# Kernel optimization log

Measured on AMD Instinct MI355X. Metric: run time of the kernel, lower is better.

Reference implementation:

```python
import jax, jax.numpy as jnp
import numpy as np

B, S, HID, H = 2, 2048, 1024, 16
D_HEAD = HID // H  # 64
EPS = 1e-5


def _gammas():
    lo, hi = np.log(1.0 / 512.0), np.log(1.0 / 32.0)
    return (1.0 - np.exp(np.linspace(lo, hi, H))).astype(np.float32)


def _decay_mask():
    # D[h, n, m] = gamma_h^(n-m) for n >= m else 0  (causal exponential decay)
    gam = jnp.asarray(_gammas())                      # [H]
    pos = jnp.arange(S, dtype=jnp.float32)
    diff = pos[:, None] - pos[None, :]                # [S, S]
    keep = diff >= 0
    logg = jnp.log(gam)[:, None, None]                # [H,1,1]
    safe = jnp.where(keep, diff, 0.0)[None]           # avoid inf for masked entries
    return jnp.where(keep[None], jnp.exp(safe * logg), 0.0)  # [H, S, S]


def setup_inputs() -> dict:
    key = jax.random.key(0)
    ks = jax.random.split(key, 10)
    rn = lambda k, shape, s=1.0: jax.random.normal(k, shape, dtype=jnp.float32) * s
    return {
        "x": rn(ks[0], (B, S, HID)),
        "wq": rn(ks[1], (H, D_HEAD, D_HEAD), 1.0 / np.sqrt(D_HEAD)),
        "bq": rn(ks[2], (H, D_HEAD), 0.02),
        "wk": rn(ks[3], (H, D_HEAD, D_HEAD), 1.0 / np.sqrt(D_HEAD)),
        "bk": rn(ks[4], (H, D_HEAD), 0.02),
        "wv": rn(ks[5], (H, D_HEAD, D_HEAD), 1.0 / np.sqrt(D_HEAD)),
        "theta": rn(ks[6], (H, D_HEAD), 1.0 / D_HEAD),
        "gn_weight": jnp.ones((HID,), jnp.float32),
        "gn_bias": jnp.zeros((HID,), jnp.float32),
        "weight1": rn(ks[7], (HID, HID), 1.0 / HID),
        "weight2": rn(ks[8], (HID, HID), 1.0 / HID),
    }


def reference(x, wq, bq, wk, bk, wv, theta, gn_weight, gn_bias, weight1, weight2):
    # Per-head retention (all heads vectorized; torch loops over heads).
    xh = x.reshape(B, S, H, D_HEAD)
    q = jnp.einsum('bshd,hde->bshe', xh, wq) + bq
    k = jnp.einsum('bshd,hde->bshe', xh, wk) + bk
    v = jnp.einsum('bshd,hde->bshe', xh, wv)
    # Complex rotary factors exp(i*n*theta) on q, conj on k -> real part of q k^H:
    ang = jnp.arange(S, dtype=jnp.float32)[:, None, None] * theta[None]  # [S,H,d]
    cs, sn = jnp.cos(ang), jnp.sin(ang)
    scores = (jnp.einsum('bshd,bthd->bhst', q * cs, k * cs)
              + jnp.einsum('bshd,bthd->bhst', q * sn, k * sn))  # Re(QK^H) [B,H,S,S]
    scores = scores * _decay_mask()[None]                        # decay mask
    ret = jnp.einsum('bhst,bthd->bshd', scores, v)               # [B,S,H,d]
    # GroupNorm with groups = n_heads over channels (per-head normalization).
    mean = jnp.mean(ret, axis=-1, keepdims=True)
    var = jnp.var(ret, axis=-1, keepdims=True)
    retn = (ret - mean) * jax.lax.rsqrt(var + EPS)
    retn = retn.reshape(B, S, HID) * gn_weight + gn_bias
    # Swish gate on x @ W1, residual add, project with W2.
    gate = x @ weight1
    out = gate * jax.nn.sigmoid(gate) + retn
    return out @ weight2
```

## Files before the change

### kernel.cpp

```cpp
#include <hip/hip_runtime.h>
#include <cstdint>
#include <cstddef>

#define B_ 2
#define S_ 2048
#define HID_ 1024
#define H_ 16
#define DH_ 64

typedef __attribute__((ext_vector_type(8))) short short8;
typedef __attribute__((ext_vector_type(8))) unsigned short ushort8;
typedef __attribute__((ext_vector_type(4))) unsigned short ushort4v;
typedef __attribute__((ext_vector_type(4))) float floatx4;
typedef __attribute__((ext_vector_type(4))) float float4v;

static __device__ __forceinline__ unsigned short f2bf(float f) {
  unsigned int u = __float_as_uint(f);
  u += 0x7fffu + ((u >> 16) & 1u);
  return (unsigned short)(u >> 16);
}
static __device__ __forceinline__ float bf2f(unsigned short h) {
  return __uint_as_float(((unsigned int)h) << 16);
}

__global__ __launch_bounds__(256) void convert_kernel(
    const float* __restrict__ x, const float* __restrict__ w1,
    const float* __restrict__ w2, unsigned short* __restrict__ x_bf,
    unsigned short* __restrict__ w1t, unsigned short* __restrict__ w2t_hi,
    unsigned short* __restrict__ w2t_lo) {
  const int NX = B_ * S_ * HID_;
  const int NW = HID_ * HID_;
  int idx = blockIdx.x * 256 + threadIdx.x;
  if (idx < NX) {
    x_bf[idx] = f2bf(x[idx]);
  } else if (idx < NX + NW) {
    int i = idx - NX;
    int n = i >> 10, k = i & 1023;
    w1t[i] = f2bf(w1[k * HID_ + n]);
  } else if (idx < NX + 2 * NW) {
    int i = idx - NX - NW;
    int n = i >> 10, k = i & 1023;
    float v = w2[k * HID_ + n];
    unsigned short h = f2bf(v);
    w2t_hi[i] = h;
    w2t_lo[i] = f2bf(v - bf2f(h));
  }
}

__global__ __launch_bounds__(256) void qkv_kernel(
    const float* __restrict__ x, const float* __restrict__ wq,
    const float* __restrict__ bq, const float* __restrict__ wk,
    const float* __restrict__ bk, const float* __restrict__ wv,
    const float* __restrict__ theta,
    unsigned short* __restrict__ q_h, unsigned short* __restrict__ q_l,
    unsigned short* __restrict__ k_h, unsigned short* __restrict__ k_l,
    unsigned short* __restrict__ v_th, unsigned short* __restrict__ v_tl,
    int b) {
  __shared__ __align__(16) float xs[64 * 68];
  __shared__ __align__(16) float wqs[64 * 68];
  __shared__ __align__(16) float wks[64 * 68];
  __shared__ __align__(16) float wvs[64 * 68];

  int tid = threadIdx.x;
  int st = blockIdx.x, h = blockIdx.y;
  int s0 = st * 64;

#pragma unroll
  for (int i = 0; i < 4; ++i) {
    int cid = tid + i * 256;
    int r = cid >> 4, c4 = (cid & 15) * 4;
    *reinterpret_cast<float4v*>(&xs[r * 68 + c4]) =
        *reinterpret_cast<const float4v*>(x + ((size_t)(b * S_ + s0 + r)) * HID_ + h * DH_ + c4);
  }
#pragma unroll
  for (int i = 0; i < 4; ++i) {
    int cid = tid + i * 256;
    int d = cid >> 4, c4 = (cid & 15) * 4;
    *reinterpret_cast<float4v*>(&wqs[d * 68 + c4]) =
        *reinterpret_cast<const float4v*>(wq + (size_t)(h * DH_ + d) * DH_ + c4);
    *reinterpret_cast<float4v*>(&wks[d * 68 + c4]) =
        *reinterpret_cast<const float4v*>(wk + (size_t)(h * DH_ + d) * DH_ + c4);
    *reinterpret_cast<float4v*>(&wvs[d * 68 + c4]) =
        *reinterpret_cast<const float4v*>(wv + (size_t)(h * DH_ + d) * DH_ + c4);
  }
  __syncthreads();

  int rg = tid >> 3;
  int cg = tid & 7;
  int r0 = rg * 2, c0 = cg * 8;

  float aq[2][8], ak[2][8], av[2][8];
#pragma unroll
  for (int i = 0; i < 2; ++i)
#pragma unroll
    for (int j = 0; j < 8; ++j) { aq[i][j] = 0.f; ak[i][j] = 0.f; av[i][j] = 0.f; }

  for (int d = 0; d < 64; ++d) {
    float x0 = xs[(r0 + 0) * 68 + d];
    float x1 = xs[(r0 + 1) * 68 + d];
#pragma unroll
    for (int j = 0; j < 8; ++j) {
      float wqv = wqs[d * 68 + c0 + j];
      float wkv = wks[d * 68 + c0 + j];
      float wvv = wvs[d * 68 + c0 + j];
      aq[0][j] += x0 * wqv; aq[1][j] += x1 * wqv;
      ak[0][j] += x0 * wkv; ak[1][j] += x1 * wkv;
      av[0][j] += x0 * wvv; av[1][j] += x1 * wvv;
    }
  }

  float thv[8], bqv[8], bkv[8];
#pragma unroll
  for (int j = 0; j < 8; ++j) {
    thv[j] = theta[h * DH_ + c0 + j];
    bqv[j] = bq[h * DH_ + c0 + j];
    bkv[j] = bk[h * DH_ + c0 + j];
  }

  __syncthreads();
  unsigned short* VtH = reinterpret_cast<unsigned short*>(xs);
  unsigned short* VtL = reinterpret_cast<unsigned short*>(wqs);

#pragma unroll
  for (int i = 0; i < 2; ++i) {
    int s = s0 + r0 + i;
    size_t qb = ((size_t)h * S_ + s) * 128;
    ushort8 qch, qcl, qsh, qsl, kch, kcl, ksh, ksl;
#pragma unroll
    for (int j = 0; j < 8; ++j) {
      float q = aq[i][j] + bqv[j];
      float k = ak[i][j] + bkv[j];
      float ang = (float)s * thv[j];
      float cs = cosf(ang), sn = sinf(ang);
      float qc = q * cs, qs = q * sn;
      unsigned short hq1 = f2bf(qc);
      qch[j] = hq1;
      qcl[j] = f2bf(qc - bf2f(hq1));
      unsigned short hq2 = f2bf(qs);
      qsh[j] = hq2;
      qsl[j] = f2bf(qs - bf2f(hq2));
      float kc = k * cs, ksn = k * sn;
      unsigned short h1 = f2bf(kc);
      kch[j] = h1;
      kcl[j] = f2bf(kc - bf2f(h1));
      unsigned short h2 = f2bf(ksn);
      ksh[j] = h2;
      ksl[j] = f2bf(ksn - bf2f(h2));
      float vv = av[i][j];
      unsigned short vh1 = f2bf(vv);
      VtH[(c0 + j) * 72 + (r0 + i)] = vh1;
      VtL[(c0 + j) * 72 + (r0 + i)] = f2bf(vv - bf2f(vh1));
    }
    *reinterpret_cast<ushort8*>(q_h + qb + c0) = qch;
    *reinterpret_cast<ushort8*>(q_h + qb + 64 + c0) = qsh;
    *reinterpret_cast<ushort8*>(q_l + qb + c0) = qcl;
    *reinterpret_cast<ushort8*>(q_l + qb + 64 + c0) = qsl;
    *reinterpret_cast<ushort8*>(k_h + qb + c0) = kch;
    *reinterpret_cast<ushort8*>(k_h + qb + 64 + c0) = ksh;
    *reinterpret_cast<ushort8*>(k_l + qb + c0) = kcl;
    *reinterpret_cast<ushort8*>(k_l + qb + 64 + c0) = ksl;
  }
  __syncthreads();
#pragma unroll
  for (int i = 0; i < 2; ++i) {
    int cid = tid + i * 256;
    int d = cid >> 3, t8 = (cid & 7) * 8;
    size_t gb = ((size_t)(h * 64 + d)) * S_ + s0 + t8;
    *reinterpret_cast<ushort8*>(v_th + gb) = *reinterpret_cast<const ushort8*>(&VtH[d * 72 + t8]);
    *reinterpret_cast<ushort8*>(v_tl + gb) = *reinterpret_cast<const ushort8*>(&VtL[d * 72 + t8]);
  }
}

#define SCOFF(row, colb)   ((row) * 256 + ((colb) ^ (((row) & 7) << 4)))

__global__ __launch_bounds__(256, 2) void retention_split_kernel(
    const unsigned short* __restrict__ q_h, const unsigned short* __restrict__ q_l,
    const unsigned short* __restrict__ k_h, const unsigned short* __restrict__ k_l,
    const unsigned short* __restrict__ v_th, const unsigned short* __restrict__ v_tl,
    float* __restrict__ partial) {
  __shared__ __align__(16) unsigned short Kh[64 * 128];
  __shared__ __align__(16) unsigned short Kl[64 * 128];
  __shared__ __align__(16) unsigned short Vh[64 * 64];
  __shared__ __align__(16) unsigned short Vl[64 * 64];
  __shared__ __align__(16) float Sc[64 * 64];

  char* KhB = (char*)Kh;
  char* KlB = (char*)Kl;
  char* VhB = (char*)Vh;
  char* VlB = (char*)Vl;
  char* ScB = (char*)Sc;

  int tid = threadIdx.x;
  int w = tid >> 6;
  int lane = tid & 63, ln = lane & 15, quad = lane >> 4;
  int f = blockIdx.x;
  int h = ((f & 7) << 1) | ((f >> 3) & 1);
  int half = (f >> 4) & 1;
  int qt = 31 - (f >> 5);
  int s0 = qt * 64;
  int prow = quad * 4;

  int m = (qt + 2) >> 1;
  int kt0 = half ? m : 0;
  int kt1 = half ? (qt + 1) : m;

  const float lo_c = -6.2383246250395075f, hi_c = -3.4657359027997265f;
  float gam = 1.f - __expf(lo_c + (hi_c - lo_c) * ((float)h * (1.f / 15.f)));
  float logg = __logf(gam);

  float rowf[4], colf[4];
#pragma unroll
  for (int rr = 0; rr < 4; ++rr)
    rowf[rr] = __expf((float)(w * 16 + prow + rr) * logg);
#pragma unroll
  for (int ns = 0; ns < 4; ++ns)
    colf[ns] = __expf(-(float)(ns * 16 + ln) * logg);

  const unsigned short* khb = k_h + (size_t)h * S_ * 128;
  const unsigned short* klb = k_l + (size_t)h * S_ * 128;
  const unsigned short* vhb = v_th + (size_t)h * 64 * S_;
  const unsigned short* vlb = v_tl + (size_t)h * 64 * S_;

  int sQ = s0 + w * 16 + ln;
  const unsigned short* qhp = q_h + ((size_t)h * S_ + sQ) * 128 + quad * 8;
  const unsigned short* qlp = q_l + ((size_t)h * S_ + sQ) * 128 + quad * 8;
  short8 qfh[4], qfl[4];
#pragma unroll
  for (int c = 0; c < 4; ++c) {
    qfh[c] = *reinterpret_cast<const short8*>(qhp + c * 32);
    qfl[c] = *reinterpret_cast<const short8*>(qlp + c * 32);
  }

  floatx4 accO[4];
#pragma unroll
  for (int i = 0; i < 4; ++i) accO[i] = (floatx4){0.f, 0.f, 0.f, 0.f};

  ushort8 skh[4], skl[4], svh[2], svl[2];
  int t00 = kt0 * 64;
#pragma unroll
  for (int i = 0; i < 4; ++i) {
    int cid = tid + i * 256;
    int r = cid >> 4, c8 = (cid & 15) * 8;
    skh[i] = *reinterpret_cast<const ushort8*>(khb + ((size_t)(t00 + r)) * 128 + c8);
    skl[i] = *reinterpret_cast<const ushort8*>(klb + ((size_t)(t00 + r)) * 128 + c8);
  }
#pragma unroll
  for (int i = 0; i < 2; ++i) {
    int cid = tid + i * 256;
    int d = cid >> 3, t8 = (cid & 7) * 8;
    svh[i] = *reinterpret_cast<const ushort8*>(vhb + (size_t)d * S_ + t00 + t8);
    svl[i] = *reinterpret_cast<const ushort8*>(vlb + (size_t)d * S_ + t00 + t8);
  }
#pragma unroll
  for (int i = 0; i < 4; ++i) {
    int cid = tid + i * 256;
    int r = cid >> 4;
    int ko = r * 256 + (((cid & 15) * 16) ^ ((r & 7) << 4));
    *reinterpret_cast<ushort8*>(KhB + ko) = skh[i];
    *reinterpret_cast<ushort8*>(KlB + ko) = skl[i];
  }
#pragma unroll
  for (int i = 0; i < 2; ++i) {
    int cid = tid + i * 256;
    int d = cid >> 3;
    int vo = d * 128 + (((cid & 7) * 16) ^ ((d & 7) << 4));
    *reinterpret_cast<ushort8*>(VhB + vo) = svh[i];
    *reinterpret_cast<ushort8*>(VlB + vo) = svl[i];
  }
  if (kt0 + 1 < kt1) {
    int t01 = (kt0 + 1) * 64;
#pragma unroll
    for (int i = 0; i < 4; ++i) {
      int cid = tid + i * 256;
      int r = cid >> 4, c8 = (cid & 15) * 8;
      skh[i] = *reinterpret_cast<const ushort8*>(khb + ((size_t)(t01 + r)) * 128 + c8);
      skl[i] = *reinterpret_cast<const ushort8*>(klb + ((size_t)(t01 + r)) * 128 + c8);
    }
#pragma unroll
    for (int i = 0; i < 2; ++i) {
      int cid = tid + i * 256;
      int d = cid >> 3, t8 = (cid & 7) * 8;
      svh[i] = *reinterpret_cast<const ushort8*>(vhb + (size_t)d * S_ + t01 + t8);
      svl[i] = *reinterpret_cast<const ushort8*>(vlb + (size_t)d * S_ + t01 + t8);
    }
  }
  __syncthreads();

  for (int kt = kt0; kt < kt1; ++kt) {
    floatx4 accS[4];
#pragma unroll
    for (int ns = 0; ns < 4; ++ns) {
      floatx4 a = (floatx4){0.f, 0.f, 0.f, 0.f};
      int row = ns * 16 + ln;
#pragma unroll
      for (int ks = 0; ks < 4; ++ks) {
        int off = row * 256 + ((ks * 64 + quad * 16) ^ ((ln & 7) << 4));
        short8 kh = *reinterpret_cast<const short8*>(KhB + off);
        short8 kl = *reinterpret_cast<const short8*>(KlB + off);
        a = __builtin_amdgcn_mfma_f32_16x16x32_bf16(qfh[ks], kh, a, 0, 0, 0);
        a = __builtin_amdgcn_mfma_f32_16x16x32_bf16(qfl[ks], kh, a, 0, 0, 0);
        a = __builtin_amdgcn_mfma_f32_16x16x32_bf16(qfh[ks], kl, a, 0, 0, 0);
      }
      accS[ns] = a;
    }

    float tf = __expf((float)(64 * (qt - kt)) * logg);
    float trf[4];
#pragma unroll
    for (int rr = 0; rr < 4; ++rr) trf[rr] = tf * rowf[rr];
    if (kt < qt) {
#pragma unroll
      for (int ns = 0; ns < 4; ++ns) {
        int col = ns * 16 + ln;
#pragma unroll
        for (int rr = 0; rr < 4; ++rr) {
          int row = w * 16 + prow + rr;
          *reinterpret_cast<float*>(ScB + SCOFF(row, col * 4)) =
              accS[ns][rr] * trf[rr] * colf[ns];
        }
      }
    } else {
#pragma unroll
      for (int ns = 0; ns < 4; ++ns) {
        int col = ns * 16 + ln;
#pragma unroll
        for (int rr = 0; rr < 4; ++rr) {
          int row = w * 16 + prow + rr;
          float v = accS[ns][rr] * trf[rr] * colf[ns];
          *reinterpret_cast<float*>(ScB + SCOFF(row, col * 4)) =
              (row >= col) ? v : 0.f;
        }
      }
    }

#pragma unroll
    for (int ks = 0; ks < 2; ++ks) {
      int prw = w * 16 + ln;
      int cb = ks * 128 + quad * 32;
      float4v p0 = *reinterpret_cast<const float4v*>(ScB + SCOFF(prw, cb));
      float4v p1 = *reinterpret_cast<const float4v*>(ScB + SCOFF(prw, cb + 16));
      short8 ph, pl;
#pragma unroll
      for (int j = 0; j < 4; ++j) {
        unsigned short hh = f2bf(p0[j]);
        ph[j] = (short)hh;
        pl[j] = (short)f2bf(p0[j] - bf2f(hh));
        unsigned short hh2 = f2bf(p1[j]);
        ph[4 + j] = (short)hh2;
        pl[4 + j] = (short)f2bf(p1[j] - bf2f(hh2));
      }
#pragma unroll
      for (int ds = 0; ds < 4; ++ds) {
        int d = ds * 16 + ln;
        int voff = d * 128 + ((ks * 64 + quad * 16) ^ ((ln & 7) << 4));
        short8 vh = *reinterpret_cast<const short8*>(VhB + voff);
        short8 vl = *reinterpret_cast<const short8*>(VlB + voff);
        accO[ds] = __builtin_amdgcn_mfma_f32_16x16x32_bf16(ph, vh, accO[ds], 0, 0, 0);
        accO[ds] = __builtin_amdgcn_mfma_f32_16x16x32_bf16(pl, vh, accO[ds], 0, 0, 0);
        accO[ds] = __builtin_amdgcn_mfma_f32_16x16x32_bf16(ph, vl, accO[ds], 0, 0, 0);
      }
    }

    __syncthreads();
    if (kt + 1 < kt1) {
#pragma unroll
      for (int i = 0; i < 4; ++i) {
        int cid = tid + i * 256;
        int r = cid >> 4;
        int ko = r * 256 + (((cid & 15) * 16) ^ ((r & 7) << 4));
        *reinterpret_cast<ushort8*>(KhB + ko) = skh[i];
        *reinterpret_cast<ushort8*>(KlB + ko) = skl[i];
      }
#pragma unroll
      for (int i = 0; i < 2; ++i) {
        int cid = tid + i * 256;
        int d = cid >> 3;
        int vo = d * 128 + (((cid & 7) * 16) ^ ((d & 7) << 4));
        *reinterpret_cast<ushort8*>(VhB + vo) = svh[i];
        *reinterpret_cast<ushort8*>(VlB + vo) = svl[i];
      }
      if (kt + 2 < kt1) {
        int t0n = (kt + 2) * 64;
#pragma unroll
        for (int i = 0; i < 4; ++i) {
          int cid = tid + i * 256;
          int r = cid >> 4, c8 = (cid & 15) * 8;
          skh[i] = *reinterpret_cast<const ushort8*>(khb + ((size_t)(t0n + r)) * 128 + c8);
          skl[i] = *reinterpret_cast<const ushort8*>(klb + ((size_t)(t0n + r)) * 128 + c8);
        }
#pragma unroll
        for (int i = 0; i < 2; ++i) {
          int cid = tid + i * 256;
          int d = cid >> 3, t8 = (cid & 7) * 8;
          svh[i] = *reinterpret_cast<const ushort8*>(vhb + (size_t)d * S_ + t0n + t8);
          svl[i] = *reinterpret_cast<const ushort8*>(vlb + (size_t)d * S_ + t0n + t8);
        }
      }
      __syncthreads();
    }
  }

  float* pout = partial + ((size_t)(((h * 32 + qt) << 1) + half)) * 4096;
#pragma unroll
  for (int ds = 0; ds < 4; ++ds) {
#pragma unroll
    for (int rr = 0; rr < 4; ++rr) {
      pout[(w * 16 + quad * 4 + rr) * 64 + ds * 16 + ln] = accO[ds][rr];
    }
  }
}

__global__ __launch_bounds__(256) void combine_gn_kernel(
    const float* __restrict__ partial, const float* __restrict__ gn_w,
    const float* __restrict__ gn_b, float* __restrict__ retn, int b) {
  __shared__ float gnred[64][8];
  int tid = threadIdx.x;
  int qi = blockIdx.x;
  int h = qi >> 5, qt = qi & 31;
  const float* p0 = partial + (size_t)qi * 8192;
  const float* p1 = p0 + 4096;

  int r2 = tid >> 2;
  int sub = tid & 3;
  float a16[16];
#pragma unroll
  for (int c = 0; c < 4; ++c) {
    float4v va = *reinterpret_cast<const float4v*>(p0 + r2 * 64 + sub * 16 + c * 4);
    float4v vb = *reinterpret_cast<const float4v*>(p1 + r2 * 64 + sub * 16 + c * 4);
#pragma unroll
    for (int j = 0; j < 4; ++j) a16[c * 4 + j] = va[j] + vb[j];
  }

  float psum = 0.f, psq = 0.f;
#pragma unroll
  for (int i = 0; i < 16; ++i) { psum += a16[i]; psq += a16[i] * a16[i]; }
  gnred[r2][sub] = psum;
  gnred[r2][4 + sub] = psq;
  float sum = gnred[r2][0] + gnred[r2][1] + gnred[r2][2] + gnred[r2][3];
  float sq = gnred[r2][4] + gnred[r2][5] + gnred[r2][6] + gnred[r2][7];
  float mean = sum * (1.f / 64.f);
  float var = sq * (1.f / 64.f) - mean * mean;
  float rstd = rsqrtf(var + 1e-5f);

  size_t obase = ((size_t)(b * S_ + qt * 64 + r2)) * HID_ + h * DH_ + sub * 16;
#pragma unroll
  for (int i = 0; i < 16; ++i) {
    float gw = gn_w[h * DH_ + sub * 16 + i];
    float gb = gn_b[h * DH_ + sub * 16 + i];
    retn[obase + i] = (a16[i] - mean) * rstd * gw + gb;
  }
}

__global__ __launch_bounds__(256) void gemm_gate_kernel(
    const unsigned short* __restrict__ A, const unsigned short* __restrict__ Bt,
    const float* __restrict__ retn, unsigned short* __restrict__ pre_hi,
    unsigned short* __restrict__ pre_lo) {
  const int K = HID_;
  __shared__ __align__(16) unsigned short Al[128 * 56];
  __shared__ __align__(16) unsigned short Bl[128 * 56];

  int tid = threadIdx.x;
  int lane = tid & 63, ln = lane & 15, quad = lane >> 4;
  int w = tid >> 6, wm = w >> 1, wn = w & 1;
  int m0 = blockIdx.y * 128, n0 = blockIdx.x * 128;

  floatx4 acc[4][4];
#pragma unroll
  for (int i = 0; i < 4; ++i)
#pragma unroll
    for (int j = 0; j < 4; ++j) acc[i][j] = (floatx4){0.f, 0.f, 0.f, 0.f};

  for (int k0 = 0; k0 < K; k0 += 32) {
    __syncthreads();
#pragma unroll
    for (int i = 0; i < 2; ++i) {
      int cid = tid + i * 256;
      int r = cid >> 2, c8 = (cid & 3) * 8;
      *reinterpret_cast<ushort8*>(&Al[r * 56 + c8]) =
          *reinterpret_cast<const ushort8*>(A + (size_t)(m0 + r) * K + k0 + c8);
      *reinterpret_cast<ushort8*>(&Bl[r * 56 + c8]) =
          *reinterpret_cast<const ushort8*>(Bt + (size_t)(n0 + r) * K + k0 + c8);
    }
    __syncthreads();

    short8 af[4], bfr[4];
#pragma unroll
    for (int i = 0; i < 4; ++i) {
      af[i] = *reinterpret_cast<const short8*>(&Al[(wm * 64 + i * 16 + ln) * 56 + quad * 8]);
      bfr[i] = *reinterpret_cast<const short8*>(&Bl[(wn * 64 + i * 16 + ln) * 56 + quad * 8]);
    }
#pragma unroll
    for (int mi = 0; mi < 4; ++mi)
#pragma unroll
      for (int ni = 0; ni < 4; ++ni)
        acc[mi][ni] = __builtin_amdgcn_mfma_f32_16x16x32_bf16(af[mi], bfr[ni], acc[mi][ni], 0, 0, 0);
  }

#pragma unroll
  for (int mi = 0; mi < 4; ++mi) {
#pragma unroll
    for (int r = 0; r < 4; ++r) {
      int row = m0 + wm * 64 + mi * 16 + quad * 4 + r;
#pragma unroll
      for (int ni = 0; ni < 4; ++ni) {
        int col = n0 + wn * 64 + ni * 16 + ln;
        float g = acc[mi][ni][r];
        float val = g * (1.f / (1.f + __expf(-g))) + retn[(size_t)row * HID_ + col];
        unsigned short hh = f2bf(val);
        size_t oidx = (size_t)row * HID_ + col;
        pre_hi[oidx] = hh;
        pre_lo[oidx] = f2bf(val - bf2f(hh));
      }
    }
  }
}

__global__ __launch_bounds__(256) void gemm_out_kernel(
    const unsigned short* __restrict__ Ah, const unsigned short* __restrict__ Alo,
    const unsigned short* __restrict__ Bth, const unsigned short* __restrict__ Btlo,
    float* __restrict__ out_f) {
  const int K = HID_;
  __shared__ __align__(16) unsigned short AhS[128 * 56];
  __shared__ __align__(16) unsigned short AlS[128 * 56];
  __shared__ __align__(16) unsigned short BhS[128 * 56];
  __shared__ __align__(16) unsigned short BlS[128 * 56];

  int tid = threadIdx.x;
  int lane = tid & 63, ln = lane & 15, quad = lane >> 4;
  int w = tid >> 6, wm = w >> 1, wn = w & 1;
  int m0 = blockIdx.y * 128, n0 = blockIdx.x * 128;

  floatx4 acc[4][4];
#pragma unroll
  for (int i = 0; i < 4; ++i)
#pragma unroll
    for (int j = 0; j < 4; ++j) acc[i][j] = (floatx4){0.f, 0.f, 0.f, 0.f};

  for (int k0 = 0; k0 < K; k0 += 32) {
    __syncthreads();
#pragma unroll
    for (int i = 0; i < 2; ++i) {
      int cid = tid + i * 256;
      int r = cid >> 2, c8 = (cid & 3) * 8;
      size_t ga = (size_t)(m0 + r) * K + k0 + c8;
      size_t gb = (size_t)(n0 + r) * K + k0 + c8;
      *reinterpret_cast<ushort8*>(&AhS[r * 56 + c8]) = *reinterpret_cast<const ushort8*>(Ah + ga);
      *reinterpret_cast<ushort8*>(&AlS[r * 56 + c8]) = *reinterpret_cast<const ushort8*>(Alo + ga);
      *reinterpret_cast<ushort8*>(&BhS[r * 56 + c8]) = *reinterpret_cast<const ushort8*>(Bth + gb);
      *reinterpret_cast<ushort8*>(&BlS[r * 56 + c8]) = *reinterpret_cast<const ushort8*>(Btlo + gb);
    }
    __syncthreads();

    short8 afh[4], afl[4], bfh[4], bfl[4];
#pragma unroll
    for (int i = 0; i < 4; ++i) {
      int ao = (wm * 64 + i * 16 + ln) * 56 + quad * 8;
      int bo = (wn * 64 + i * 16 + ln) * 56 + quad * 8;
      afh[i] = *reinterpret_cast<const short8*>(&AhS[ao]);
      afl[i] = *reinterpret_cast<const short8*>(&AlS[ao]);
      bfh[i] = *reinterpret_cast<const short8*>(&BhS[bo]);
      bfl[i] = *reinterpret_cast<const short8*>(&BlS[bo]);
    }
#pragma unroll
    for (int mi = 0; mi < 4; ++mi)
#pragma unroll
      for (int ni = 0; ni < 4; ++ni) {
        floatx4 a = acc[mi][ni];
        a = __builtin_amdgcn_mfma_f32_16x16x32_bf16(afh[mi], bfh[ni], a, 0, 0, 0);
        a = __builtin_amdgcn_mfma_f32_16x16x32_bf16(afl[mi], bfh[ni], a, 0, 0, 0);
        a = __builtin_amdgcn_mfma_f32_16x16x32_bf16(afh[mi], bfl[ni], a, 0, 0, 0);
        acc[mi][ni] = a;
      }
  }

#pragma unroll
  for (int mi = 0; mi < 4; ++mi) {
#pragma unroll
    for (int r = 0; r < 4; ++r) {
      int row = m0 + wm * 64 + mi * 16 + quad * 4 + r;
#pragma unroll
      for (int ni = 0; ni < 4; ++ni) {
        int col = n0 + wn * 64 + ni * 16 + ln;
        out_f[(size_t)row * HID_ + col] = acc[mi][ni][r];
      }
    }
  }
}

extern "C" void kernel_launch(void* const* d_in, const int* in_sizes, int n_in,
                              void* d_out, int out_size, void* d_ws,
                              size_t ws_size, hipStream_t stream) {
  (void)in_sizes; (void)n_in; (void)out_size; (void)ws_size;
  const float* x = (const float*)d_in[0];
  const float* wq = (const float*)d_in[1];
  const float* bq = (const float*)d_in[2];
  const float* wk = (const float*)d_in[3];
  const float* bk = (const float*)d_in[4];
  const float* wv = (const float*)d_in[5];
  const float* theta = (const float*)d_in[6];
  const float* gn_w = (const float*)d_in[7];
  const float* gn_b = (const float*)d_in[8];
  const float* w1 = (const float*)d_in[9];
  const float* w2 = (const float*)d_in[10];

  const size_t MB = 1024 * 1024;
  char* ws = (char*)d_ws;
  unsigned short* x_bf   = (unsigned short*)(ws + 0 * MB);
  unsigned short* w1t    = (unsigned short*)(ws + 8 * MB);
  unsigned short* w2t_hi = (unsigned short*)(ws + 10 * MB);
  unsigned short* w2t_lo = (unsigned short*)(ws + 12 * MB);
  unsigned short* q_h    = (unsigned short*)(ws + 14 * MB);
  unsigned short* q_l    = (unsigned short*)(ws + 22 * MB);
  unsigned short* k_h    = (unsigned short*)(ws + 30 * MB);
  unsigned short* k_l    = (unsigned short*)(ws + 38 * MB);
  unsigned short* v_th   = (unsigned short*)(ws + 46 * MB);
  unsigned short* v_tl   = (unsigned short*)(ws + 50 * MB);
  float*          retn   = (float*)(ws + 54 * MB);
  float*          partial= (float*)(ws + 70 * MB);
  unsigned short* pre_hi = (unsigned short*)(ws + 14 * MB);
  unsigned short* pre_lo = (unsigned short*)(ws + 22 * MB);
  float* out = (float*)d_out;

  convert_kernel<<<dim3(24576), 256, 0, stream>>>(x, w1, w2, x_bf, w1t, w2t_hi, w2t_lo);
  for (int b = 0; b < B_; ++b) {
    qkv_kernel<<<dim3(S_ / 64, H_), 256, 0, stream>>>(
        x, wq, bq, wk, bk, wv, theta, q_h, q_l, k_h, k_l, v_th, v_tl, b);
    retention_split_kernel<<<dim3(1024), 256, 0, stream>>>(
        q_h, q_l, k_h, k_l, v_th, v_tl, partial);
    combine_gn_kernel<<<dim3(512), 256, 0, stream>>>(
        partial, gn_w, gn_b, retn, b);
  }
  gemm_gate_kernel<<<dim3(HID_ / 128, (B_ * S_) / 128), 256, 0, stream>>>(
      x_bf, w1t, retn, pre_hi, pre_lo);
  gemm_out_kernel<<<dim3(HID_ / 128, (B_ * S_) / 128), 256, 0, stream>>>(
      pre_hi, pre_lo, w2t_hi, w2t_lo, out);
}
```

Before: 345.4 us.

## Split retention into quarter key ranges with 32-wide key tiles; halve GEMM N tiles

The retention kernel now splits each query tile's causal key range into four parts instead of two and uses 32-row key tiles, launching twice as many blocks with half the shared memory so four blocks can share a CU. The combine kernel sums four partials instead of two. Both output GEMMs move from 128x128 to 128x64 tiles to double their grid size. The aim is better CU occupancy and load balance, at the cost of more partial-sum traffic, more synchronisation per unit of work and less operand reuse in the GEMMs.

Result: slower. 366.6 us (+6.1%).

```diff
diff --git a/kernel.cpp b/kernel.cpp
--- a/kernel.cpp
+++ b/kernel.cpp
@@ -171,18 +171,18 @@
   }
 }
 
-#define SCOFF(row, colb)   ((row) * 256 + ((colb) ^ (((row) & 7) << 4)))
-
-__global__ __launch_bounds__(256, 2) void retention_split_kernel(
+#define SCOFF(row, colb)   ((row) * 128 + ((colb) ^ (((row) & 7) << 4)))
+
+__global__ __launch_bounds__(256, 4) void retention_q_kernel(
     const unsigned short* __restrict__ q_h, const unsigned short* __restrict__ q_l,
     const unsigned short* __restrict__ k_h, const unsigned short* __restrict__ k_l,
     const unsigned short* __restrict__ v_th, const unsigned short* __restrict__ v_tl,
     float* __restrict__ partial) {
-  __shared__ __align__(16) unsigned short Kh[64 * 128];
-  __shared__ __align__(16) unsigned short Kl[64 * 128];
+  __shared__ __align__(16) unsigned short Kh[32 * 128];
+  __shared__ __align__(16) unsigned short Kl[32 * 128];
   __shared__ __align__(16) unsigned short Vh[64 * 64];
   __shared__ __align__(16) unsigned short Vl[64 * 64];
-  __shared__ __align__(16) float Sc[64 * 64];
+  __shared__ __align__(16) float Sc[64 * 32];
 
   char* KhB = (char*)Kh;
   char* KlB = (char*)Kl;
@@ -195,25 +195,25 @@
   int lane = tid & 63, ln = lane & 15, quad = lane >> 4;
   int f = blockIdx.x;
   int h = ((f & 7) << 1) | ((f >> 3) & 1);
-  int half = (f >> 4) & 1;
-  int qt = 31 - (f >> 5);
+  int quarter = (f >> 4) & 3;
+  int qt = 31 - (f >> 6);
   int s0 = qt * 64;
   int prow = quad * 4;
 
-  int m = (qt + 2) >> 1;
-  int kt0 = half ? m : 0;
-  int kt1 = half ? (qt + 1) : m;
+  int T = 2 * qt + 2;
+  int kt0 = (quarter * T) >> 2;
+  int kt1 = ((quarter + 1) * T) >> 2;
 
   const float lo_c = -6.2383246250395075f, hi_c = -3.4657359027997265f;
   float gam = 1.f - __expf(lo_c + (hi_c - lo_c) * ((float)h * (1.f / 15.f)));
   float logg = __logf(gam);
 
-  float rowf[4], colf[4];
+  float rowf[4], colf[2];
 #pragma unroll
   for (int rr = 0; rr < 4; ++rr)
     rowf[rr] = __expf((float)(w * 16 + prow + rr) * logg);
 #pragma unroll
-  for (int ns = 0; ns < 4; ++ns)
+  for (int ns = 0; ns < 2; ++ns)
     colf[ns] = __expf(-(float)(ns * 16 + ln) * logg);
 
   const unsigned short* khb = k_h + (size_t)h * S_ * 128;
@@ -235,61 +235,55 @@
 #pragma unroll
   for (int i = 0; i < 4; ++i) accO[i] = (floatx4){0.f, 0.f, 0.f, 0.f};
 
-  ushort8 skh[4], skl[4], svh[2], svl[2];
-  int t00 = kt0 * 64;
-#pragma unroll
-  for (int i = 0; i < 4; ++i) {
-    int cid = tid + i * 256;
-    int r = cid >> 4, c8 = (cid & 15) * 8;
-    skh[i] = *reinterpret_cast<const ushort8*>(khb + ((size_t)(t00 + r)) * 128 + c8);
-    skl[i] = *reinterpret_cast<const ushort8*>(klb + ((size_t)(t00 + r)) * 128 + c8);
-  }
-#pragma unroll
-  for (int i = 0; i < 2; ++i) {
-    int cid = tid + i * 256;
-    int d = cid >> 3, t8 = (cid & 7) * 8;
-    svh[i] = *reinterpret_cast<const ushort8*>(vhb + (size_t)d * S_ + t00 + t8);
-    svl[i] = *reinterpret_cast<const ushort8*>(vlb + (size_t)d * S_ + t00 + t8);
-  }
-#pragma unroll
-  for (int i = 0; i < 4; ++i) {
-    int cid = tid + i * 256;
-    int r = cid >> 4;
-    int ko = r * 256 + (((cid & 15) * 16) ^ ((r & 7) << 4));
-    *reinterpret_cast<ushort8*>(KhB + ko) = skh[i];
-    *reinterpret_cast<ushort8*>(KlB + ko) = skl[i];
-  }
-#pragma unroll
-  for (int i = 0; i < 2; ++i) {
-    int cid = tid + i * 256;
-    int d = cid >> 3;
-    int vo = d * 128 + (((cid & 7) * 16) ^ ((d & 7) << 4));
-    *reinterpret_cast<ushort8*>(VhB + vo) = svh[i];
-    *reinterpret_cast<ushort8*>(VlB + vo) = svl[i];
-  }
-  if (kt0 + 1 < kt1) {
-    int t01 = (kt0 + 1) * 64;
-#pragma unroll
-    for (int i = 0; i < 4; ++i) {
+  ushort8 skh[2], skl[2], svh, svl;
+  {
+    int t00 = kt0 * 32;
+#pragma unroll
+    for (int i = 0; i < 2; ++i) {
       int cid = tid + i * 256;
       int r = cid >> 4, c8 = (cid & 15) * 8;
-      skh[i] = *reinterpret_cast<const ushort8*>(khb + ((size_t)(t01 + r)) * 128 + c8);
-      skl[i] = *reinterpret_cast<const ushort8*>(klb + ((size_t)(t01 + r)) * 128 + c8);
+      skh[i] = *reinterpret_cast<const ushort8*>(khb + ((size_t)(t00 + r)) * 128 + c8);
+      skl[i] = *reinterpret_cast<const ushort8*>(klb + ((size_t)(t00 + r)) * 128 + c8);
+    }
+    {
+      int d = tid >> 2, t8 = (tid & 3) * 8;
+      svh = *reinterpret_cast<const ushort8*>(vhb + (size_t)d * S_ + t00 + t8);
+      svl = *reinterpret_cast<const ushort8*>(vlb + (size_t)d * S_ + t00 + t8);
     }
 #pragma unroll
     for (int i = 0; i < 2; ++i) {
       int cid = tid + i * 256;
-      int d = cid >> 3, t8 = (cid & 7) * 8;
-      svh[i] = *reinterpret_cast<const ushort8*>(vhb + (size_t)d * S_ + t01 + t8);
-      svl[i] = *reinterpret_cast<const ushort8*>(vlb + (size_t)d * S_ + t01 + t8);
+      int r = cid >> 4;
+      int ko = r * 256 + (((cid & 15) * 16) ^ ((r & 7) << 4));
+      *reinterpret_cast<ushort8*>(KhB + ko) = skh[i];
+      *reinterpret_cast<ushort8*>(KlB + ko) = skl[i];
+    }
+    {
+      int d = tid >> 2;
+      int vo = d * 128 + (((tid & 3) * 16) ^ ((d & 7) << 4));
+      *reinterpret_cast<ushort8*>(VhB + vo) = svh;
+      *reinterpret_cast<ushort8*>(VlB + vo) = svl;
+    }
+    if (kt0 + 1 < kt1) {
+      int t01 = (kt0 + 1) * 32;
+#pragma unroll
+      for (int i = 0; i < 2; ++i) {
+        int cid = tid + i * 256;
+        int r = cid >> 4, c8 = (cid & 15) * 8;
+        skh[i] = *reinterpret_cast<const ushort8*>(khb + ((size_t)(t01 + r)) * 128 + c8);
+        skl[i] = *reinterpret_cast<const ushort8*>(klb + ((size_t)(t01 + r)) * 128 + c8);
+      }
+      int d = tid >> 2, t8 = (tid & 3) * 8;
+      svh = *reinterpret_cast<const ushort8*>(vhb + (size_t)d * S_ + t01 + t8);
+      svl = *reinterpret_cast<const ushort8*>(vlb + (size_t)d * S_ + t01 + t8);
     }
   }
   __syncthreads();
 
   for (int kt = kt0; kt < kt1; ++kt) {
-    floatx4 accS[4];
-#pragma unroll
-    for (int ns = 0; ns < 4; ++ns) {
+    floatx4 accS[2];
+#pragma unroll
+    for (int ns = 0; ns < 2; ++ns) {
       floatx4 a = (floatx4){0.f, 0.f, 0.f, 0.f};
       int row = ns * 16 + ln;
 #pragma unroll
@@ -304,13 +298,13 @@
       accS[ns] = a;
     }
 
-    float tf = __expf((float)(64 * (qt - kt)) * logg);
+    float tf = __expf((float)(64 * qt - 32 * kt) * logg);
     float trf[4];
 #pragma unroll
     for (int rr = 0; rr < 4; ++rr) trf[rr] = tf * rowf[rr];
-    if (kt < qt) {
-#pragma unroll
-      for (int ns = 0; ns < 4; ++ns) {
+    if (kt < 2 * qt) {
+#pragma unroll
+      for (int ns = 0; ns < 2; ++ns) {
         int col = ns * 16 + ln;
 #pragma unroll
         for (int rr = 0; rr < 4; ++rr) {
@@ -320,25 +314,24 @@
         }
       }
     } else {
-#pragma unroll
-      for (int ns = 0; ns < 4; ++ns) {
+      int off32 = 32 * (kt - 2 * qt);
+#pragma unroll
+      for (int ns = 0; ns < 2; ++ns) {
         int col = ns * 16 + ln;
 #pragma unroll
         for (int rr = 0; rr < 4; ++rr) {
           int row = w * 16 + prow + rr;
           float v = accS[ns][rr] * trf[rr] * colf[ns];
           *reinterpret_cast<float*>(ScB + SCOFF(row, col * 4)) =
-              (row >= col) ? v : 0.f;
+              (row >= col + off32) ? v : 0.f;
         }
       }
     }
 
-#pragma unroll
-    for (int ks = 0; ks < 2; ++ks) {
+    {
       int prw = w * 16 + ln;
-      int cb = ks * 128 + quad * 32;
-      float4v p0 = *reinterpret_cast<const float4v*>(ScB + SCOFF(prw, cb));
-      float4v p1 = *reinterpret_cast<const float4v*>(ScB + SCOFF(prw, cb + 16));
+      float4v p0 = *reinterpret_cast<const float4v*>(ScB + SCOFF(prw, quad * 32));
+      float4v p1 = *reinterpret_cast<const float4v*>(ScB + SCOFF(prw, quad * 32 + 16));
       short8 ph, pl;
 #pragma unroll
       for (int j = 0; j < 4; ++j) {
@@ -352,7 +345,7 @@
 #pragma unroll
       for (int ds = 0; ds < 4; ++ds) {
         int d = ds * 16 + ln;
-        int voff = d * 128 + ((ks * 64 + quad * 16) ^ ((ln & 7) << 4));
+        int voff = d * 128 + ((quad * 16) ^ ((ln & 7) << 4));
         short8 vh = *reinterpret_cast<const short8*>(VhB + voff);
         short8 vl = *reinterpret_cast<const short8*>(VlB + voff);
         accO[ds] = __builtin_amdgcn_mfma_f32_16x16x32_bf16(ph, vh, accO[ds], 0, 0, 0);
@@ -364,43 +357,37 @@
     __syncthreads();
     if (kt + 1 < kt1) {
 #pragma unroll
-      for (int i = 0; i < 4; ++i) {
+      for (int i = 0; i < 2; ++i) {
         int cid = tid + i * 256;
         int r = cid >> 4;
         int ko = r * 256 + (((cid & 15) * 16) ^ ((r & 7) << 4));
         *reinterpret_cast<ushort8*>(KhB + ko) = skh[i];
         *reinterpret_cast<ushort8*>(KlB + ko) = skl[i];
       }
-#pragma unroll
-      for (int i = 0; i < 2; ++i) {
-        int cid = tid + i * 256;
-        int d = cid >> 3;
-        int vo = d * 128 + (((cid & 7) * 16) ^ ((d & 7) << 4));
-        *reinterpret_cast<ushort8*>(VhB + vo) = svh[i];
-        *reinterpret_cast<ushort8*>(VlB + vo) = svl[i];
+      {
+        int d = tid >> 2;
+        int vo = d * 128 + (((tid & 3) * 16) ^ ((d & 7) << 4));
+        *reinterpret_cast<ushort8*>(VhB + vo) = svh;
+        *reinterpret_cast<ushort8*>(VlB + vo) = svl;
       }
       if (kt + 2 < kt1) {
-        int t0n = (kt + 2) * 64;
-#pragma unroll
-        for (int i = 0; i < 4; ++i) {
+        int t0n = (kt + 2) * 32;
+#pragma unroll
+        for (int i = 0; i < 2; ++i) {
           int cid = tid + i * 256;
           int r = cid >> 4, c8 = (cid & 15) * 8;
           skh[i] = *reinterpret_cast<const ushort8*>(khb + ((size_t)(t0n + r)) * 128 + c8);
           skl[i] = *reinterpret_cast<const ushort8*>(klb + ((size_t)(t0n + r)) * 128 + c8);
         }
-#pragma unroll
-        for (int i = 0; i < 2; ++i) {
-          int cid = tid + i * 256;
-          int d = cid >> 3, t8 = (cid & 7) * 8;
-          svh[i] = *reinterpret_cast<const ushort8*>(vhb + (size_t)d * S_ + t0n + t8);
-          svl[i] = *reinterpret_cast<const ushort8*>(vlb + (size_t)d * S_ + t0n + t8);
-        }
+        int d = tid >> 2, t8 = (tid & 3) * 8;
+        svh = *reinterpret_cast<const ushort8*>(vhb + (size_t)d * S_ + t0n + t8);
+        svl = *reinterpret_cast<const ushort8*>(vlb + (size_t)d * S_ + t0n + t8);
       }
       __syncthreads();
     }
   }
 
-  float* pout = partial + ((size_t)(((h * 32 + qt) << 1) + half)) * 4096;
+  float* pout = partial + ((size_t)((h * 32 + qt) * 4 + quarter)) * 4096;
 #pragma unroll
   for (int ds = 0; ds < 4; ++ds) {
 #pragma unroll
@@ -417,18 +404,20 @@
   int tid = threadIdx.x;
   int qi = blockIdx.x;
   int h = qi >> 5, qt = qi & 31;
-  const float* p0 = partial + (size_t)qi * 8192;
-  const float* p1 = p0 + 4096;
+  const float* p = partial + (size_t)qi * 16384;
 
   int r2 = tid >> 2;
   int sub = tid & 3;
   float a16[16];
 #pragma unroll
   for (int c = 0; c < 4; ++c) {
-    float4v va = *reinterpret_cast<const float4v*>(p0 + r2 * 64 + sub * 16 + c * 4);
-    float4v vb = *reinterpret_cast<const float4v*>(p1 + r2 * 64 + sub * 16 + c * 4);
-#pragma unroll
-    for (int j = 0; j < 4; ++j) a16[c * 4 + j] = va[j] + vb[j];
+    int o = r2 * 64 + sub * 16 + c * 4;
+    float4v v0 = *reinterpret_cast<const float4v*>(p + o);
+    float4v v1 = *reinterpret_cast<const float4v*>(p + 4096 + o);
+    float4v v2 = *reinterpret_cast<const float4v*>(p + 8192 + o);
+    float4v v3 = *reinterpret_cast<const float4v*>(p + 12288 + o);
+#pragma unroll
+    for (int j = 0; j < 4; ++j) a16[c * 4 + j] = (v0[j] + v1[j]) + (v2[j] + v3[j]);
   }
 
   float psum = 0.f, psq = 0.f;
@@ -457,18 +446,18 @@
     unsigned short* __restrict__ pre_lo) {
   const int K = HID_;
   __shared__ __align__(16) unsigned short Al[128 * 56];
-  __shared__ __align__(16) unsigned short Bl[128 * 56];
+  __shared__ __align__(16) unsigned short Bl[64 * 56];
 
   int tid = threadIdx.x;
   int lane = tid & 63, ln = lane & 15, quad = lane >> 4;
   int w = tid >> 6, wm = w >> 1, wn = w & 1;
-  int m0 = blockIdx.y * 128, n0 = blockIdx.x * 128;
-
-  floatx4 acc[4][4];
+  int m0 = blockIdx.y * 128, n0 = blockIdx.x * 64;
+
+  floatx4 acc[4][2];
 #pragma unroll
   for (int i = 0; i < 4; ++i)
 #pragma unroll
-    for (int j = 0; j < 4; ++j) acc[i][j] = (floatx4){0.f, 0.f, 0.f, 0.f};
+    for (int j = 0; j < 2; ++j) acc[i][j] = (floatx4){0.f, 0.f, 0.f, 0.f};
 
   for (int k0 = 0; k0 < K; k0 += 32) {
     __syncthreads();
@@ -478,21 +467,25 @@
       int r = cid >> 2, c8 = (cid & 3) * 8;
       *reinterpret_cast<ushort8*>(&Al[r * 56 + c8]) =
           *reinterpret_cast<const ushort8*>(A + (size_t)(m0 + r) * K + k0 + c8);
+    }
+    {
+      int r = tid >> 2, c8 = (tid & 3) * 8;
       *reinterpret_cast<ushort8*>(&Bl[r * 56 + c8]) =
           *reinterpret_cast<const ushort8*>(Bt + (size_t)(n0 + r) * K + k0 + c8);
     }
     __syncthreads();
 
-    short8 af[4], bfr[4];
-#pragma unroll
-    for (int i = 0; i < 4; ++i) {
+    short8 af[4], bfr[2];
+#pragma unroll
+    for (int i = 0; i < 4; ++i)
       af[i] = *reinterpret_cast<const short8*>(&Al[(wm * 64 + i * 16 + ln) * 56 + quad * 8]);
-      bfr[i] = *reinterpret_cast<const short8*>(&Bl[(wn * 64 + i * 16 + ln) * 56 + quad * 8]);
-    }
+#pragma unroll
+    for (int i = 0; i < 2; ++i)
+      bfr[i] = *reinterpret_cast<const short8*>(&Bl[(wn * 32 + i * 16 + ln) * 56 + quad * 8]);
 #pragma unroll
     for (int mi = 0; mi < 4; ++mi)
 #pragma unroll
-      for (int ni = 0; ni < 4; ++ni)
+      for (int ni = 0; ni < 2; ++ni)
         acc[mi][ni] = __builtin_amdgcn_mfma_f32_16x16x32_bf16(af[mi], bfr[ni], acc[mi][ni], 0, 0, 0);
   }
 
@@ -502,8 +495,8 @@
     for (int r = 0; r < 4; ++r) {
       int row = m0 + wm * 64 + mi * 16 + quad * 4 + r;
 #pragma unroll
-      for (int ni = 0; ni < 4; ++ni) {
-        int col = n0 + wn * 64 + ni * 16 + ln;
+      for (int ni = 0; ni < 2; ++ni) {
+        int col = n0 + wn * 32 + ni * 16 + ln;
         float g = acc[mi][ni][r];
         float val = g * (1.f / (1.f + __expf(-g))) + retn[(size_t)row * HID_ + col];
         unsigned short hh = f2bf(val);
@@ -522,19 +515,19 @@
   const int K = HID_;
   __shared__ __align__(16) unsigned short AhS[128 * 56];
   __shared__ __align__(16) unsigned short AlS[128 * 56];
-  __shared__ __align__(16) unsigned short BhS[128 * 56];
-  __shared__ __align__(16) unsigned short BlS[128 * 56];
+  __shared__ __align__(16) unsigned short BhS[64 * 56];
+  __shared__ __align__(16) unsigned short BlS[64 * 56];
 
   int tid = threadIdx.x;
   int lane = tid & 63, ln = lane & 15, quad = lane >> 4;
   int w = tid >> 6, wm = w >> 1, wn = w & 1;
-  int m0 = blockIdx.y * 128, n0 = blockIdx.x * 128;
-
-  floatx4 acc[4][4];
+  int m0 = blockIdx.y * 128, n0 = blockIdx.x * 64;
+
+  floatx4 acc[4][2];
 #pragma unroll
   for (int i = 0; i < 4; ++i)
 #pragma unroll
-    for (int j = 0; j < 4; ++j) acc[i][j] = (floatx4){0.f, 0.f, 0.f, 0.f};
+    for (int j = 0; j < 2; ++j) acc[i][j] = (floatx4){0.f, 0.f, 0.f, 0.f};
 
   for (int k0 = 0; k0 < K; k0 += 32) {
     __syncthreads();
@@ -543,28 +536,34 @@
       int cid = tid + i * 256;
       int r = cid >> 2, c8 = (cid & 3) * 8;
       size_t ga = (size_t)(m0 + r) * K + k0 + c8;
-      size_t gb = (size_t)(n0 + r) * K + k0 + c8;
       *reinterpret_cast<ushort8*>(&AhS[r * 56 + c8]) = *reinterpret_cast<const ushort8*>(Ah + ga);
       *reinterpret_cast<ushort8*>(&AlS[r * 56 + c8]) = *reinterpret_cast<const ushort8*>(Alo + ga);
+    }
+    {
+      int r = tid >> 2, c8 = (tid & 3) * 8;
+      size_t gb = (size_t)(n0 + r) * K + k0 + c8;
       *reinterpret_cast<ushort8*>(&BhS[r * 56 + c8]) = *reinterpret_cast<const ushort8*>(Bth + gb);
       *reinterpret_cast<ushort8*>(&BlS[r * 56 + c8]) = *reinterpret_cast<const ushort8*>(Btlo + gb);
     }
     __syncthreads();
 
-    short8 afh[4], afl[4], bfh[4], bfl[4];
+    short8 afh[4], afl[4], bfh[2], bfl[2];
 #pragma unroll
     for (int i = 0; i < 4; ++i) {
       int ao = (wm * 64 + i * 16 + ln) * 56 + quad * 8;
-      int bo = (wn * 64 + i * 16 + ln) * 56 + quad * 8;
       afh[i] = *reinterpret_cast<const short8*>(&AhS[ao]);
       afl[i] = *reinterpret_cast<const short8*>(&AlS[ao]);
+    }
+#pragma unroll
+    for (int i = 0; i < 2; ++i) {
+      int bo = (wn * 32 + i * 16 + ln) * 56 + quad * 8;
       bfh[i] = *reinterpret_cast<const short8*>(&BhS[bo]);
       bfl[i] = *reinterpret_cast<const short8*>(&BlS[bo]);
     }
 #pragma unroll
     for (int mi = 0; mi < 4; ++mi)
 #pragma unroll
-      for (int ni = 0; ni < 4; ++ni) {
+      for (int ni = 0; ni < 2; ++ni) {
         floatx4 a = acc[mi][ni];
         a = __builtin_amdgcn_mfma_f32_16x16x32_bf16(afh[mi], bfh[ni], a, 0, 0, 0);
         a = __builtin_amdgcn_mfma_f32_16x16x32_bf16(afl[mi], bfh[ni], a, 0, 0, 0);
@@ -579,8 +578,8 @@
     for (int r = 0; r < 4; ++r) {
       int row = m0 + wm * 64 + mi * 16 + quad * 4 + r;
 #pragma unroll
-      for (int ni = 0; ni < 4; ++ni) {
-        int col = n0 + wn * 64 + ni * 16 + ln;
+      for (int ni = 0; ni < 2; ++ni) {
+        int col = n0 + wn * 32 + ni * 16 + ln;
         out_f[(size_t)row * HID_ + col] = acc[mi][ni][r];
       }
     }
@@ -625,13 +624,13 @@
   for (int b = 0; b < B_; ++b) {
     qkv_kernel<<<dim3(S_ / 64, H_), 256, 0, stream>>>(
         x, wq, bq, wk, bk, wv, theta, q_h, q_l, k_h, k_l, v_th, v_tl, b);
-    retention_split_kernel<<<dim3(1024), 256, 0, stream>>>(
+    retention_q_kernel<<<dim3(2048), 256, 0, stream>>>(
         q_h, q_l, k_h, k_l, v_th, v_tl, partial);
     combine_gn_kernel<<<dim3(512), 256, 0, stream>>>(
         partial, gn_w, gn_b, retn, b);
   }
-  gemm_gate_kernel<<<dim3(HID_ / 128, (B_ * S_) / 128), 256, 0, stream>>>(
+  gemm_gate_kernel<<<dim3(HID_ / 64, (B_ * S_) / 128), 256, 0, stream>>>(
       x_bf, w1t, retn, pre_hi, pre_lo);
-  gemm_out_kernel<<<dim3(HID_ / 128, (B_ * S_) / 128), 256, 0, stream>>>(
+  gemm_out_kernel<<<dim3(HID_ / 64, (B_ * S_) / 128), 256, 0, stream>>>(
       pre_hi, pre_lo, w2t_hi, w2t_lo, out);
 }
```
